# Kernel optimization log

Measured on AMD Instinct MI355X. Metric: run time of the kernel, lower is better.

## Reference

```python
import jax, jax.numpy as jnp
import numpy as np

M, K, N = 8192, 4096, 4096

def _quantize_symmetric(t):
    # per-tensor symmetric int8 quantization: scale = max|t| / 127
    scale = jnp.max(jnp.abs(t)) / 127.0
    q = jnp.clip(jnp.round(t / scale), -127.0, 127.0).astype(jnp.int8)
    return q, scale


def setup_inputs() -> dict:
    key = jax.random.key(0)
    kx, kw, kb = jax.random.split(key, 3)
    x = jax.random.normal(kx, (M, K), dtype=jnp.float32)
    weight = jax.random.normal(kw, (N, K), dtype=jnp.float32)
    bias = jax.random.normal(kb, (N,), dtype=jnp.float32)
    return {"x": x, "weight": weight, "bias": bias}


def reference(x, weight, bias):
    # dynamic per-tensor quantization of activations and (pre-quantized) weight
    x_q, x_scale = _quantize_symmetric(x)
    w_q, w_scale = _quantize_symmetric(weight)
    # int8 GEMM with int32 accumulation (padding in the source is a no-op mathematically)
    acc = jnp.matmul(x_q.astype(jnp.int32), w_q.astype(jnp.int32).T)  # [M, N]
    # dequantize with product of per-tensor scales, then bias add
    out = acc.astype(jnp.float32) * (x_scale * w_scale) + bias
    return out
```

## Files before the change

kernel.cpp:

```cpp
#include <hip/hip_runtime.h>
#include <stdint.h>

#define MDIM 8192
#define KDIM 4096
#define NDIM 4096

typedef int v4i __attribute__((ext_vector_type(4)));

__global__ __launch_bounds__(256) void absmax2_kernel(const float* __restrict__ x,
                                                      const float* __restrict__ w,
                                                      unsigned* __restrict__ bits) {
    __shared__ float smax[4];
    const float4* src;
    int idx, stride, n4;
    unsigned* slot;
    if (blockIdx.x < 1024) {
        src = (const float4*)x;
        idx = blockIdx.x * 256 + threadIdx.x;
        stride = 1024 * 256;
        n4 = MDIM * KDIM / 4;
        slot = bits;
    } else {
        src = (const float4*)w;
        idx = (blockIdx.x - 1024) * 256 + threadIdx.x;
        stride = 512 * 256;
        n4 = NDIM * KDIM / 4;
        slot = bits + 1;
    }
    float m = 0.0f;
    for (int i = idx; i < n4; i += 4 * stride) {
        float4 a = src[i];
        float4 b = src[i + stride];
        float4 c = src[i + 2 * stride];
        float4 d = src[i + 3 * stride];
        m = fmaxf(m, fmaxf(fmaxf(fabsf(a.x), fabsf(a.y)), fmaxf(fabsf(a.z), fabsf(a.w))));
        m = fmaxf(m, fmaxf(fmaxf(fabsf(b.x), fabsf(b.y)), fmaxf(fabsf(b.z), fabsf(b.w))));
        m = fmaxf(m, fmaxf(fmaxf(fabsf(c.x), fabsf(c.y)), fmaxf(fabsf(c.z), fabsf(c.w))));
        m = fmaxf(m, fmaxf(fmaxf(fabsf(d.x), fabsf(d.y)), fmaxf(fabsf(d.z), fabsf(d.w))));
    }
#pragma unroll
    for (int off = 32; off > 0; off >>= 1)
        m = fmaxf(m, __shfl_down(m, off, 64));
    if ((threadIdx.x & 63) == 0) smax[threadIdx.x >> 6] = m;
    __syncthreads();
    if (threadIdx.x == 0) {
        float bm = fmaxf(fmaxf(smax[0], smax[1]), fmaxf(smax[2], smax[3]));
        atomicMax(slot, __float_as_uint(bm));
    }
}

__global__ __launch_bounds__(256) void quant2_kernel(const float* __restrict__ x,
                                                     const float* __restrict__ w,
                                                     const unsigned* __restrict__ bits,
                                                     int* __restrict__ xq,
                                                     int* __restrict__ wq) {
    const float4* src;
    int idx, stride, n4;
    int* dst;
    float amax;
    if (blockIdx.x < 2048) {
        src = (const float4*)x;
        idx = blockIdx.x * 256 + threadIdx.x;
        stride = 2048 * 256;
        n4 = MDIM * KDIM / 4;
        dst = xq;
        amax = __uint_as_float(bits[0]);
    } else {
        src = (const float4*)w;
        idx = (blockIdx.x - 2048) * 256 + threadIdx.x;
        stride = 1024 * 256;
        n4 = NDIM * KDIM / 4;
        dst = wq;
        amax = __uint_as_float(bits[1]);
    }
    const float scale = (amax > 0.0f) ? (amax / 127.0f) : 1.0f;
    for (int i = idx; i < n4; i += 4 * stride) {
        float4 v[4];
        v[0] = src[i];
        v[1] = src[i + stride];
        v[2] = src[i + 2 * stride];
        v[3] = src[i + 3 * stride];
#pragma unroll
        for (int u = 0; u < 4; ++u) {
            int a = __float2int_rn(v[u].x / scale);
            int b = __float2int_rn(v[u].y / scale);
            int c = __float2int_rn(v[u].z / scale);
            int d = __float2int_rn(v[u].w / scale);
            a = min(127, max(-127, a));
            b = min(127, max(-127, b));
            c = min(127, max(-127, c));
            d = min(127, max(-127, d));
            dst[i + u * stride] =
                (a & 0xFF) | ((b & 0xFF) << 8) | ((c & 0xFF) << 16) | ((d & 0xFF) << 24);
        }
    }
}

__global__ __launch_bounds__(512, 2) void gemm_i8(
    const signed char* __restrict__ Aq,
    const signed char* __restrict__ Wq,
    const float* __restrict__ bias,
    const unsigned* __restrict__ bits,
    float* __restrict__ out) {
    __shared__ __align__(16) signed char As[2 * 32768];
    __shared__ __align__(16) signed char Bs[2 * 32768];

    const int tid  = threadIdx.x;
    const int lane = tid & 63;
    const int wave = tid >> 6;
    const int wm = wave >> 2;
    const int wn = wave & 3;
    const int l15 = lane & 15;
    const int l4  = lane >> 4;
    const int swz = l15 & 7;

    const int m0 = blockIdx.y * 256;
    const int n0 = blockIdx.x * 256;

    const int srow = tid >> 3;
    const int scol = ((tid & 7) ^ (srow & 7)) << 4;
    const signed char* aSrc[4];
    const signed char* bSrc[4];
#pragma unroll
    for (int u = 0; u < 4; ++u) {
        aSrc[u] = Aq + (size_t)(m0 + u * 64 + srow) * KDIM + scol;
        bSrc[u] = Wq + (size_t)(n0 + u * 64 + srow) * KDIM + scol;
    }
    const int ldsOff = tid * 16;

    v4i acc[8][4] = {};
    v4i af[4][2], bf[2][2];

#define STAGE_FULL(BUF, KB) do {                                                          \
    _Pragma("unroll") for (int u = 0; u < 4; ++u)                                         \
        __builtin_amdgcn_global_load_lds(                                                 \
            (const __attribute__((address_space(1))) void*)(aSrc[u] + (KB)),              \
            (__attribute__((address_space(3))) void*)(As + (BUF)*32768 + u*8192 + ldsOff),\
            16, 0, 0);                                                                    \
    _Pragma("unroll") for (int u = 0; u < 4; ++u)                                         \
        __builtin_amdgcn_global_load_lds(                                                 \
            (const __attribute__((address_space(1))) void*)(bSrc[u] + (KB)),              \
            (__attribute__((address_space(3))) void*)(Bs + (BUF)*32768 + u*8192 + ldsOff),\
            16, 0, 0);                                                                    \
} while (0)

#define LDA(dst, BUF, i, kk) dst = *(const v4i*)(As + (BUF)*32768 +                       \
        (wm*128 + (i)*16 + l15)*128 + (((((kk)<<2) | l4) ^ swz) << 4))
#define LDB(dst, BUF, j, kk) dst = *(const v4i*)(Bs + (BUF)*32768 +                       \
        (wn*64 + (j)*16 + l15)*128 + (((((kk)<<2) | l4) ^ swz) << 4))

#define MFMA8(I0, J0) do {                                                                \
    _Pragma("unroll") for (int kk = 0; kk < 2; ++kk)                                      \
    _Pragma("unroll") for (int i = 0; i < 4; ++i)                                         \
    _Pragma("unroll") for (int j = 0; j < 2; ++j)                                         \
        acc[(I0)+i][(J0)+j] = __builtin_amdgcn_mfma_i32_16x16x64_i8(                      \
            af[i][kk], bf[j][kk], acc[(I0)+i][(J0)+j], 0, 0, 0);                          \
} while (0)

#define BAR() do { __builtin_amdgcn_s_barrier(); asm volatile("" ::: "memory"); } while (0)

#define TILE(BUF, DO_STAGE, NKB) do {                                                     \
               \
    if (DO_STAGE) STAGE_FULL(1 - (BUF), NKB);                                             \
    _Pragma("unroll") for (int i = 0; i < 4; ++i) { LDA(af[i][0], BUF, i, 0);             \
                                                    LDA(af[i][1], BUF, i, 1); }           \
    _Pragma("unroll") for (int j = 0; j < 2; ++j) { LDB(bf[j][0], BUF, j, 0);             \
                                                    LDB(bf[j][1], BUF, j, 1); }           \
    __builtin_amdgcn_s_setprio(1); MFMA8(0, 0); __builtin_amdgcn_s_setprio(0);            \
    BAR();                                                                                \
                                       \
    _Pragma("unroll") for (int j = 0; j < 2; ++j) { LDB(bf[j][0], BUF, 2 + j, 0);         \
                                                    LDB(bf[j][1], BUF, 2 + j, 1); }       \
    __builtin_amdgcn_s_setprio(1); MFMA8(0, 2); __builtin_amdgcn_s_setprio(0);            \
    BAR();                                                                                \
                                       \
    _Pragma("unroll") for (int i = 0; i < 4; ++i) { LDA(af[i][0], BUF, 4 + i, 0);         \
                                                    LDA(af[i][1], BUF, 4 + i, 1); }       \
    __builtin_amdgcn_s_setprio(1); MFMA8(4, 2); __builtin_amdgcn_s_setprio(0);            \
    BAR();                                                                                \
                         \
    _Pragma("unroll") for (int j = 0; j < 2; ++j) { LDB(bf[j][0], BUF, j, 0);             \
                                                    LDB(bf[j][1], BUF, j, 1); }           \
    __builtin_amdgcn_s_setprio(1); MFMA8(4, 0); __builtin_amdgcn_s_setprio(0);            \
    asm volatile("s_waitcnt vmcnt(0)" ::: "memory");                                      \
    BAR();                                                                                \
} while (0)

    STAGE_FULL(0, 0);
    asm volatile("s_waitcnt vmcnt(0)" ::: "memory");
    BAR();

#pragma unroll 1
    for (int kb = 0; kb < KDIM; kb += 256) {
        TILE(0, true, kb + 128);
        TILE(1, (kb + 256) < KDIM, kb + 256);
    }

    const float ax = __uint_as_float(bits[0]);
    const float aw = __uint_as_float(bits[1]);
    const float s = (ax / 127.0f) * (aw / 127.0f);

#pragma unroll
    for (int j = 0; j < 4; ++j) {
        const int col = n0 + wn * 64 + j * 16 + l15;
        const float bcol = bias[col];
#pragma unroll
        for (int i = 0; i < 8; ++i) {
            const int row0 = m0 + wm * 128 + i * 16 + l4 * 4;
#pragma unroll
            for (int r = 0; r < 4; ++r)
                out[(size_t)(row0 + r) * NDIM + col] = (float)acc[i][j][r] * s + bcol;
        }
    }
#undef STAGE_FULL
#undef LDA
#undef LDB
#undef MFMA8
#undef BAR
#undef TILE
}

extern "C" void kernel_launch(void* const* d_in, const int* in_sizes, int n_in,
                              void* d_out, int out_size, void* d_ws, size_t ws_size,
                              hipStream_t stream) {
    const float* x    = (const float*)d_in[0];
    const float* w    = (const float*)d_in[1];
    const float* bias = (const float*)d_in[2];
    float* out = (float*)d_out;

    unsigned* bits = (unsigned*)d_ws;
    signed char* xq = (signed char*)d_ws + 64;
    signed char* wq = xq + (size_t)MDIM * KDIM;

    hipMemsetAsync(d_ws, 0, 64, stream);

    absmax2_kernel<<<1536, 256, 0, stream>>>(x, w, bits);
    quant2_kernel<<<3072, 256, 0, stream>>>(x, w, bits, (int*)xq, (int*)wq);

    dim3 grid(NDIM / 256, MDIM / 256);
    gemm_i8<<<grid, 512, 0, stream>>>(xq, wq, bias, bits, out);
}
```

Measured before the change: 481.6 us.

## Split global-to-LDS staging into quarter chunks interleaved across MFMA phases

Restructures the GEMM main loop so each K tile's global-to-LDS loads are broken into half-tile A/B chunks and issued across the four MFMA phases. Chunks of the next tile are written into the current buffer as soon as the regions they overwrite have been read into registers. Partial vmcnt waits replace the full drain, and explicit lgkmcnt waits are added. The goal is a deeper, more continuous overlap of memory traffic with MFMA work, at the cost of more barriers and tricky buffer-reuse correctness.

```diff
diff --git a/kernel.cpp b/kernel.cpp
--- a/kernel.cpp
+++ b/kernel.cpp
@@ -122,79 +122,90 @@
     const signed char* aSrc[4];
     const signed char* bSrc[4];
 #pragma unroll
-    for (int u = 0; u < 4; ++u) {
-        aSrc[u] = Aq + (size_t)(m0 + u * 64 + srow) * KDIM + scol;
-        bSrc[u] = Wq + (size_t)(n0 + u * 64 + srow) * KDIM + scol;
-    }
-    const int ldsOff = tid * 16;
+    for (int c = 0; c < 4; ++c) {
+        aSrc[c] = Aq + (size_t)(m0 + c * 64 + srow) * KDIM + scol;
+        bSrc[c] = Wq + (size_t)(n0 + c * 64 + srow) * KDIM + scol;
+    }
+    const int ldst = tid * 16;
 
     v4i acc[8][4] = {};
-    v4i af[4][2], bf[2][2];
-
-#define STAGE_FULL(BUF, KB) do {                                                          \
-    _Pragma("unroll") for (int u = 0; u < 4; ++u)                                         \
-        __builtin_amdgcn_global_load_lds(                                                 \
-            (const __attribute__((address_space(1))) void*)(aSrc[u] + (KB)),              \
-            (__attribute__((address_space(3))) void*)(As + (BUF)*32768 + u*8192 + ldsOff),\
-            16, 0, 0);                                                                    \
-    _Pragma("unroll") for (int u = 0; u < 4; ++u)                                         \
-        __builtin_amdgcn_global_load_lds(                                                 \
-            (const __attribute__((address_space(1))) void*)(bSrc[u] + (KB)),              \
-            (__attribute__((address_space(3))) void*)(Bs + (BUF)*32768 + u*8192 + ldsOff),\
-            16, 0, 0);                                                                    \
-} while (0)
-
-#define LDA(dst, BUF, i, kk) dst = *(const v4i*)(As + (BUF)*32768 +                       \
-        (wm*128 + (i)*16 + l15)*128 + (((((kk)<<2) | l4) ^ swz) << 4))
-#define LDB(dst, BUF, j, kk) dst = *(const v4i*)(Bs + (BUF)*32768 +                       \
-        (wn*64 + (j)*16 + l15)*128 + (((((kk)<<2) | l4) ^ swz) << 4))
-
-#define MFMA8(I0, J0) do {                                                                \
+    v4i af[4][2], bf[4][2];
+
+#define GLL(SRC, DST) __builtin_amdgcn_global_load_lds(                                   \
+        (const __attribute__((address_space(1))) void*)(SRC),                             \
+        (__attribute__((address_space(3))) void*)(DST), 16, 0, 0)
+
+#define STG_A(BUF, h, KO) do {                                                            \
+    GLL(aSrc[(h)*2 + 0] + (KO), As + (BUF)*32768 + (h)*16384 + 0*8192 + ldst);            \
+    GLL(aSrc[(h)*2 + 1] + (KO), As + (BUF)*32768 + (h)*16384 + 1*8192 + ldst);            \
+} while (0)
+#define STG_B(BUF, h, KO) do {                                                            \
+    GLL(bSrc[(h)*2 + 0] + (KO), Bs + (BUF)*32768 + (h)*16384 + 0*8192 + ldst);            \
+    GLL(bSrc[(h)*2 + 1] + (KO), Bs + (BUF)*32768 + (h)*16384 + 1*8192 + ldst);            \
+} while (0)
+
+#define LDA(BUF, i, kk) (*(const v4i*)(As + (BUF)*32768 +                                 \
+        (wm*128 + (i)*16 + l15)*128 + (((((kk)<<2) | l4) ^ swz) << 4)))
+#define LDB(BUF, j, kk) (*(const v4i*)(Bs + (BUF)*32768 +                                 \
+        (wn*64 + (j)*16 + l15)*128 + (((((kk)<<2) | l4) ^ swz) << 4)))
+
+#define MQ(I0, J0) do {                                                                   \
     _Pragma("unroll") for (int kk = 0; kk < 2; ++kk)                                      \
     _Pragma("unroll") for (int i = 0; i < 4; ++i)                                         \
     _Pragma("unroll") for (int j = 0; j < 2; ++j)                                         \
         acc[(I0)+i][(J0)+j] = __builtin_amdgcn_mfma_i32_16x16x64_i8(                      \
-            af[i][kk], bf[j][kk], acc[(I0)+i][(J0)+j], 0, 0, 0);                          \
-} while (0)
-
-#define BAR() do { __builtin_amdgcn_s_barrier(); asm volatile("" ::: "memory"); } while (0)
-
-#define TILE(BUF, DO_STAGE, NKB) do {                                                     \
-               \
-    if (DO_STAGE) STAGE_FULL(1 - (BUF), NKB);                                             \
-    _Pragma("unroll") for (int i = 0; i < 4; ++i) { LDA(af[i][0], BUF, i, 0);             \
-                                                    LDA(af[i][1], BUF, i, 1); }           \
-    _Pragma("unroll") for (int j = 0; j < 2; ++j) { LDB(bf[j][0], BUF, j, 0);             \
-                                                    LDB(bf[j][1], BUF, j, 1); }           \
-    __builtin_amdgcn_s_setprio(1); MFMA8(0, 0); __builtin_amdgcn_s_setprio(0);            \
-    BAR();                                                                                \
-                                       \
-    _Pragma("unroll") for (int j = 0; j < 2; ++j) { LDB(bf[j][0], BUF, 2 + j, 0);         \
-                                                    LDB(bf[j][1], BUF, 2 + j, 1); }       \
-    __builtin_amdgcn_s_setprio(1); MFMA8(0, 2); __builtin_amdgcn_s_setprio(0);            \
-    BAR();                                                                                \
-                                       \
-    _Pragma("unroll") for (int i = 0; i < 4; ++i) { LDA(af[i][0], BUF, 4 + i, 0);         \
-                                                    LDA(af[i][1], BUF, 4 + i, 1); }       \
-    __builtin_amdgcn_s_setprio(1); MFMA8(4, 2); __builtin_amdgcn_s_setprio(0);            \
-    BAR();                                                                                \
-                         \
-    _Pragma("unroll") for (int j = 0; j < 2; ++j) { LDB(bf[j][0], BUF, j, 0);             \
-                                                    LDB(bf[j][1], BUF, j, 1); }           \
-    __builtin_amdgcn_s_setprio(1); MFMA8(4, 0); __builtin_amdgcn_s_setprio(0);            \
-    asm volatile("s_waitcnt vmcnt(0)" ::: "memory");                                      \
-    BAR();                                                                                \
-} while (0)
-
-    STAGE_FULL(0, 0);
-    asm volatile("s_waitcnt vmcnt(0)" ::: "memory");
+            af[i][kk], bf[(J0)+j][kk], acc[(I0)+i][(J0)+j], 0, 0, 0);                     \
+} while (0)
+
+#define BAR()   do { __builtin_amdgcn_s_barrier(); asm volatile("" ::: "memory"); } while (0)
+#define LGKM0() asm volatile("s_waitcnt lgkmcnt(0)" ::: "memory")
+#define VMC(n)  asm volatile("s_waitcnt vmcnt(" #n ")" ::: "memory")
+
+#define TILE_BODY(BUF, NBUF, KO1, KO2, ST_Q0, ST_Q123, VMQ3) do {                         \
+                       \
+    _Pragma("unroll") for (int j = 0; j < 2; ++j) {                                       \
+        bf[j][0] = LDB(BUF, j, 0); bf[j][1] = LDB(BUF, j, 1); }                           \
+    _Pragma("unroll") for (int i = 0; i < 4; ++i) {                                       \
+        af[i][0] = LDA(BUF, i, 0); af[i][1] = LDA(BUF, i, 1); }                           \
+    if (ST_Q0) STG_A(NBUF, 1, KO1);                                                       \
+    BAR(); LGKM0();                                                                       \
+    __builtin_amdgcn_s_setprio(1); MQ(0, 0); __builtin_amdgcn_s_setprio(0);               \
+    BAR();                                                                                \
+                                     \
+    _Pragma("unroll") for (int j = 0; j < 2; ++j) {                                       \
+        bf[2+j][0] = LDB(BUF, 2+j, 0); bf[2+j][1] = LDB(BUF, 2+j, 1); }                   \
+    if (ST_Q123) STG_B(BUF, 0, KO2);                                                      \
+    BAR(); LGKM0();                                                                       \
+    __builtin_amdgcn_s_setprio(1); MQ(0, 2); __builtin_amdgcn_s_setprio(0);               \
+    BAR();                                                                                \
+                 \
+    _Pragma("unroll") for (int i = 0; i < 4; ++i) {                                       \
+        af[i][0] = LDA(BUF, 4+i, 0); af[i][1] = LDA(BUF, 4+i, 1); }                       \
+    if (ST_Q123) STG_B(BUF, 1, KO2);                                                      \
+    BAR(); LGKM0();                                                                       \
+    __builtin_amdgcn_s_setprio(1); MQ(4, 0); __builtin_amdgcn_s_setprio(0);               \
+    BAR();                                                                                \
+                            \
+    if (ST_Q123) STG_A(BUF, 0, KO2);                                                      \
+    BAR();                                                                                \
+    __builtin_amdgcn_s_setprio(1); MQ(4, 2); __builtin_amdgcn_s_setprio(0);               \
+    VMQ3;                                                                                 \
+    BAR();                                                                                \
+} while (0)
+
+    STG_B(0, 0, 0); STG_B(0, 1, 0); STG_A(0, 0, 0); STG_A(0, 1, 0);
+    STG_B(1, 0, 128); STG_B(1, 1, 128); STG_A(1, 0, 128);
+    VMC(6);
     BAR();
 
 #pragma unroll 1
-    for (int kb = 0; kb < KDIM; kb += 256) {
-        TILE(0, true, kb + 128);
-        TILE(1, (kb + 256) < KDIM, kb + 256);
-    }
+    for (int kt = 0; kt < 15; ++kt) {
+        const int kb = kt * 256;
+        TILE_BODY(0, 1, kb + 128, kb + 256, 1, 1, VMC(6));
+        TILE_BODY(1, 0, kb + 256, kb + 384, 1, 1, VMC(6));
+    }
+    TILE_BODY(0, 1, 3968, 0, 1, 0, VMC(0));
+    TILE_BODY(1, 0, 0, 0, 0, 0, ((void)0));
 
     const float ax = __uint_as_float(bits[0]);
     const float aw = __uint_as_float(bits[1]);
@@ -212,12 +223,16 @@
                 out[(size_t)(row0 + r) * NDIM + col] = (float)acc[i][j][r] * s + bcol;
         }
     }
-#undef STAGE_FULL
+#undef GLL
+#undef STG_A
+#undef STG_B
 #undef LDA
 #undef LDB
-#undef MFMA8
+#undef MQ
 #undef BAR
-#undef TILE
+#undef LGKM0
+#undef VMC
+#undef TILE_BODY
 }
 
 extern "C" void kernel_launch(void* const* d_in, const int* in_sizes, int n_in,
```

Result: faster. 454.9 us (-5.6%).
